# Kernel optimization log

Hardware: AMD Instinct MI355X
Metric: run time of the kernel (lower is better)

Reference implementation:

```python
import jax, jax.numpy as jnp
import numpy as np

B, T, D = 32, 4096, 64
K = 512
COMMITMENT_COST = 0.25


def setup_inputs() -> dict:
    key = jax.random.key(0)
    kz, kw = jax.random.split(key)
    z = jax.random.normal(kz, (B, T, D), dtype=jnp.float32)
    # matches nn.init.uniform_(weight, -1/K, 1/K)
    W = jax.random.uniform(kw, (K, D), dtype=jnp.float32, minval=-1.0 / K, maxval=1.0 / K)
    return {"z": z, "W": W}


def reference(z, W):
    b, t, d = z.shape
    z_flat = z.reshape(-1, d)                                   # [N, D]
    # squared euclidean distances via ||z||^2 + ||w||^2 - 2 z.w
    dist = (jnp.sum(z_flat * z_flat, axis=1, keepdims=True)
            + jnp.sum(W * W, axis=1)
            - 2.0 * z_flat @ W.T)                               # [N, K]
    indices = jnp.argmin(dist, axis=1)                          # [N]
    z_q = W[indices].reshape(b, t, d)                           # gather
    # straight-through estimator
    z_q_st = z + jax.lax.stop_gradient(z_q - z)
    loss = COMMITMENT_COST * jnp.mean((z - jax.lax.stop_gradient(z_q_st)) ** 2)
    return z_q_st, indices.reshape(b, t), loss
```

## Files before the change

### kernel.cpp

```cpp
#include <hip/hip_runtime.h>
#include <hip/hip_bf16.h>
#include <math.h>

#define NROWS 131072
#define KC    512
#define DD    64
#define NELEM (NROWS * DD)

#define OUT_IDX_OFF  NELEM
#define OUT_LOSS_OFF (NELEM + NROWS)

#define MARGIN 3e-5f

#define WSO_CNT   0
#define WSO_DONE  4
#define WSO_LOSS  8
#define WSO_WNORM 64
#define WSO_BH    4096
#define WSO_BL    (WSO_BH + 65536)
#define WSO_LIST  (WSO_BL + 65536)

typedef __attribute__((ext_vector_type(8))) short short8;
typedef __attribute__((ext_vector_type(4))) float f32x4;

__device__ __forceinline__ short f2bf_bits(float f) {
  __hip_bfloat16 h = __float2bfloat16(f);
  short s; __builtin_memcpy(&s, &h, 2); return s;
}
__device__ __forceinline__ float bfbits2f(short s) {
  __hip_bfloat16 h; __builtin_memcpy(&h, &s, 2);
  return __bfloat162float(h);
}
__device__ __forceinline__ void cvt8(const float* __restrict__ p, short8& hi, short8& lo) {
#pragma unroll
  for (int j = 0; j < 8; j++) {
    float f = p[j];
    short hb = f2bf_bits(f);
    float r = f - bfbits2f(hb);
    hi[j] = hb;
    lo[j] = f2bf_bits(r);
  }
}

__device__ __forceinline__ float np_sumsq64(const float* __restrict__ p) {
#pragma clang fp contract(off)
  float r0 = p[0] * p[0], r1 = p[1] * p[1], r2 = p[2] * p[2], r3 = p[3] * p[3];
  float r4 = p[4] * p[4], r5 = p[5] * p[5], r6 = p[6] * p[6], r7 = p[7] * p[7];
  for (int i = 8; i < 64; i += 8) {
    r0 = r0 + p[i + 0] * p[i + 0];
    r1 = r1 + p[i + 1] * p[i + 1];
    r2 = r2 + p[i + 2] * p[i + 2];
    r3 = r3 + p[i + 3] * p[i + 3];
    r4 = r4 + p[i + 4] * p[i + 4];
    r5 = r5 + p[i + 5] * p[i + 5];
    r6 = r6 + p[i + 6] * p[i + 6];
    r7 = r7 + p[i + 7] * p[i + 7];
  }
  return ((r0 + r1) + (r2 + r3)) + ((r4 + r5) + (r6 + r7));
}

__global__ void k_prep(const float* __restrict__ W, short8* __restrict__ Bh,
                       short8* __restrict__ Bl, float* __restrict__ wnorm,
                       int* __restrict__ flagCnt, int* __restrict__ doneCnt,
                       float* __restrict__ lossSum) {
  int gtid = blockIdx.x * blockDim.x + threadIdx.x;
  if (gtid == 0) { *flagCnt = 0; *doneCnt = 0; *lossSum = 0.0f; }
  int t = gtid >> 7, rem = gtid & 127;
  int h = rem >> 6, L = rem & 63;
  int cw = (t << 4) + (L & 15);
  int dbase = (h << 5) + ((L >> 4) << 3);
  short8 hi, lo;
  cvt8(W + (cw << 6) + dbase, hi, lo);
  Bh[gtid] = hi;
  Bl[gtid] = lo;
  if (gtid < KC) wnorm[gtid] = np_sumsq64(W + (gtid << 6));
}

#define MT 2
#define ROWS_PER_WAVE (MT * 16)
#define ROWS_PER_BLOCK (ROWS_PER_WAVE * 4)

__global__ __launch_bounds__(256, 4) void k_screen(
    const float* __restrict__ z, const float* __restrict__ W,
    const short8* __restrict__ Bh, const short8* __restrict__ Bl,
    const float* __restrict__ wnorm, float* __restrict__ out,
    int* __restrict__ flagList, int* __restrict__ flagCnt,
    float* __restrict__ lossSum) {
  const int lane = threadIdx.x & 63;
  const int wave = threadIdx.x >> 6;
  const int rowBase = blockIdx.x * ROWS_PER_BLOCK + wave * ROWS_PER_WAVE;
  const int m = lane & 15, quad = lane >> 4;

  short8 Ah[MT][2], Al[MT][2];
#pragma unroll
  for (int mt = 0; mt < MT; mt++) {
    const float* zp = z + (size_t)(rowBase + (mt << 4) + m) * DD + (quad << 3);
#pragma unroll
    for (int h = 0; h < 2; h++) cvt8(zp + (h << 5), Ah[mt][h], Al[mt][h]);
  }

  float b1[MT][4], b2[MT][4];
  int bi[MT][4];
#pragma unroll
  for (int mt = 0; mt < MT; mt++)
#pragma unroll
    for (int r = 0; r < 4; r++) { b1[mt][r] = 1e30f; b2[mt][r] = 1e30f; bi[mt][r] = 0; }

  short8 cBh[2], cBl[2];
#pragma unroll
  for (int h = 0; h < 2; h++) {
    cBh[h] = Bh[(h << 6) + lane];
    cBl[h] = Bl[(h << 6) + lane];
  }
  float cwn = wnorm[m];

  for (int t = 0; t < 32; t++) {
    const int tn = (t + 1) & 31;
    short8 nBh[2], nBl[2];
#pragma unroll
    for (int h = 0; h < 2; h++) {
      nBh[h] = Bh[(((tn << 1) + h) << 6) + lane];
      nBl[h] = Bl[(((tn << 1) + h) << 6) + lane];
    }
    float nwn = wnorm[(tn << 4) + m];

    f32x4 acc[MT] = {{0.f, 0.f, 0.f, 0.f}, {0.f, 0.f, 0.f, 0.f}};
#pragma unroll
    for (int h = 0; h < 2; h++) {
#pragma unroll
      for (int mt = 0; mt < MT; mt++)
        acc[mt] = __builtin_amdgcn_mfma_f32_16x16x32_bf16(Ah[mt][h], cBh[h], acc[mt], 0, 0, 0);
#pragma unroll
      for (int mt = 0; mt < MT; mt++)
        acc[mt] = __builtin_amdgcn_mfma_f32_16x16x32_bf16(Al[mt][h], cBh[h], acc[mt], 0, 0, 0);
#pragma unroll
      for (int mt = 0; mt < MT; mt++)
        acc[mt] = __builtin_amdgcn_mfma_f32_16x16x32_bf16(Ah[mt][h], cBl[h], acc[mt], 0, 0, 0);
    }

    int colv = (t << 4) + m;
#pragma unroll
    for (int mt = 0; mt < MT; mt++)
#pragma unroll
      for (int r = 0; r < 4; r++) {
        float s = fmaf(-2.0f, acc[mt][r], cwn);
        if (s < b1[mt][r]) { b2[mt][r] = b1[mt][r]; b1[mt][r] = s; bi[mt][r] = colv; }
        else b2[mt][r] = fminf(b2[mt][r], s);
      }

    cBh[0] = nBh[0]; cBh[1] = nBh[1];
    cBl[0] = nBl[0]; cBl[1] = nBl[1];
    cwn = nwn;
  }

#pragma unroll
  for (int off = 1; off < 16; off <<= 1) {
#pragma unroll
    for (int mt = 0; mt < MT; mt++)
#pragma unroll
      for (int r = 0; r < 4; r++) {
        float o1 = __shfl_xor(b1[mt][r], off, 64);
        float o2 = __shfl_xor(b2[mt][r], off, 64);
        int oi = __shfl_xor(bi[mt][r], off, 64);
        if (o1 < b1[mt][r] || (o1 == b1[mt][r] && oi < bi[mt][r])) {
          b2[mt][r] = fminf(b1[mt][r], o2);
          b1[mt][r] = o1; bi[mt][r] = oi;
        } else {
          b2[mt][r] = fminf(b2[mt][r], o1);
        }
      }
  }

  float lossAcc = 0.f;
#pragma unroll
  for (int mt = 0; mt < MT; mt++)
#pragma unroll
    for (int r = 0; r < 4; r++) {
      const int row = rowBase + (mt << 4) + (quad << 2) + r;
      const int ki = bi[mt][r];
      f32x4 zv = *(const f32x4*)(z + (size_t)row * DD + (m << 2));
      f32x4 wv = *(const f32x4*)(W + (ki << 6) + (m << 2));
      f32x4 ov;
#pragma unroll
      for (int j = 0; j < 4; j++) {
        float tt = wv[j] - zv[j];
        ov[j] = zv[j] + tt;
        float dl = zv[j] - ov[j];
        lossAcc = fmaf(dl, dl, lossAcc);
      }
      *(f32x4*)(out + (size_t)row * DD + (m << 2)) = ov;
      if (m == 0) {
        out[OUT_IDX_OFF + row] = (float)ki;
        if (b2[mt][r] - b1[mt][r] < MARGIN) {
          int slot = atomicAdd(flagCnt, 1);
          flagList[slot] = row;
        }
      }
    }

#pragma unroll
  for (int off = 1; off < 64; off <<= 1) lossAcc += __shfl_xor(lossAcc, off, 64);
  if (lane == 0) atomicAdd(lossSum, lossAcc);
}

__global__ void k_refine(const float* __restrict__ z, const float* __restrict__ W,
                         const float* __restrict__ wnp, float* __restrict__ out,
                         const int* __restrict__ flagList,
                         const int* __restrict__ flagCnt,
                         float* __restrict__ lossSum, int* __restrict__ doneCnt) {
  int nflag = *flagCnt;
  int lane = threadIdx.x & 63;
  int wave = (blockIdx.x * blockDim.x + threadIdx.x) >> 6;
  int nWaves = (gridDim.x * blockDim.x) >> 6;

  for (int f = wave; f < nflag; f += nWaves) {
    int row = flagList[f];
    const float* zr = z + (size_t)row * DD;
    float A = np_sumsq64(zr);

    float best = 1e30f;
    int bk = 0x7fffffff;
#pragma unroll
    for (int j = 0; j < KC / 64; j++) {
      int k = lane + (j << 6);
      const float* wk = W + (k << 6);
      double cd = 0.0;
      for (int d = 0; d < DD; d++) cd = fma((double)zr[d], (double)wk[d], cd);
      float twoC = (float)(2.0 * cd);
      float dist;
      {
#pragma clang fp contract(off)
        float t1 = A + wnp[k];
        dist = t1 - twoC;
      }
      if (dist < best || (dist == best && k < bk)) { best = dist; bk = k; }
    }
#pragma unroll
    for (int off = 1; off < 64; off <<= 1) {
      float ov = __shfl_xor(best, off, 64);
      int ok = __shfl_xor(bk, off, 64);
      if (ov < best || (ov == best && ok < bk)) { best = ov; bk = ok; }
    }

    int kold = (int)out[OUT_IDX_OFF + row];
    if (bk != kold) {
      float zv = zr[lane];
      float wN = W[(bk << 6) + lane];
      float oOld = out[(size_t)row * DD + lane];
      float tN = wN - zv;
      float oN = zv + tN;
      out[(size_t)row * DD + lane] = oN;
      float dN = zv - oN, dO = zv - oOld;
      float delta = dN * dN - dO * dO;
#pragma unroll
      for (int off = 1; off < 64; off <<= 1) delta += __shfl_xor(delta, off, 64);
      if (lane == 0) {
        atomicAdd(lossSum, delta);
        out[OUT_IDX_OFF + row] = (float)bk;
      }
    }
  }

  __syncthreads();
  if (threadIdx.x == 0) {
    __threadfence();
    int d = atomicAdd(doneCnt, 1);
    if (d == (int)gridDim.x - 1) {
      float s = atomicAdd(lossSum, 0.0f);
      out[OUT_LOSS_OFF] = 0.25f * s / (float)NELEM;
    }
  }
}

extern "C" void kernel_launch(void* const* d_in, const int* in_sizes, int n_in,
                              void* d_out, int out_size, void* d_ws, size_t ws_size,
                              hipStream_t stream) {
  const float* z = (const float*)d_in[0];
  const float* W = (const float*)d_in[1];
  float* out = (float*)d_out;
  char* ws = (char*)d_ws;

  int* flagCnt = (int*)(ws + WSO_CNT);
  int* doneCnt = (int*)(ws + WSO_DONE);
  float* lossSum = (float*)(ws + WSO_LOSS);
  float* wnorm = (float*)(ws + WSO_WNORM);
  short8* Bh = (short8*)(ws + WSO_BH);
  short8* Bl = (short8*)(ws + WSO_BL);
  int* flagList = (int*)(ws + WSO_LIST);

  k_prep<<<16, 256, 0, stream>>>(W, Bh, Bl, wnorm, flagCnt, doneCnt, lossSum);
  k_screen<<<NROWS / ROWS_PER_BLOCK, 256, 0, stream>>>(z, W, Bh, Bl, wnorm, out,
                                                       flagList, flagCnt, lossSum);
  k_refine<<<256, 256, 0, stream>>>(z, W, wnorm, out, flagList, flagCnt,
                                    lossSum, doneCnt);
}
```

Baseline: 202.8 us.

## Split codebook across waves and share row tile via LDS in screen kernel

Each block now handles 64 rows, staged once into shared memory as hi/lo bf16 fragments. Each of the four waves scans a quarter of the codebook (8 tiles) over all 64 rows, rather than every wave scanning all 512 codes for its own 32 rows. Per-wave best and second-best results are merged through shared memory, and the per-block loss is reduced before a single atomic. This cuts per-wave B-fragment traffic and atomics and raises MT, at the cost of extra syncs, more LDS and register pressure, and a tie-break merge that no longer prefers the lower index on equal distances.

Result: slower. 491.6 us (+142.4%).

```diff
diff --git a/kernel.cpp b/kernel.cpp
--- a/kernel.cpp
+++ b/kernel.cpp
@@ -76,28 +76,52 @@
   if (gtid < KC) wnorm[gtid] = np_sumsq64(W + (gtid << 6));
 }
 
-#define MT 2
-#define ROWS_PER_WAVE (MT * 16)
-#define ROWS_PER_BLOCK (ROWS_PER_WAVE * 4)
-
-__global__ __launch_bounds__(256, 4) void k_screen(
+#define MT 4
+#define ROWS_PER_BLOCK 64
+#define TPW 8
+
+__global__ __launch_bounds__(256, 6) void k_screen(
     const float* __restrict__ z, const float* __restrict__ W,
     const short8* __restrict__ Bh, const short8* __restrict__ Bl,
     const float* __restrict__ wnorm, float* __restrict__ out,
     int* __restrict__ flagList, int* __restrict__ flagCnt,
     float* __restrict__ lossSum) {
-  const int lane = threadIdx.x & 63;
-  const int wave = threadIdx.x >> 6;
-  const int rowBase = blockIdx.x * ROWS_PER_BLOCK + wave * ROWS_PER_WAVE;
+  const int tid = threadIdx.x;
+  const int lane = tid & 63;
+  const int wave = tid >> 6;
+  const int rowBase = blockIdx.x * ROWS_PER_BLOCK;
   const int m = lane & 15, quad = lane >> 4;
 
+  __shared__ short8 sAh[MT * 2][64];
+  __shared__ short8 sAl[MT * 2][64];
+  __shared__ float sb1[4][64], sb2[4][64];
+  __shared__ int   sbi[4][64];
+  __shared__ float lw[4];
+
+  {
+    const int row = tid >> 2;
+    const int colbase = (tid & 3) << 4;
+    const int mt = row >> 4, mm = row & 15;
+    const int h = colbase >> 5;
+    const int q0 = (colbase >> 3) & 3;
+    const float* zp = z + (size_t)(rowBase + row) * DD + colbase;
+    short8 hi0, lo0, hi1, lo1;
+    cvt8(zp, hi0, lo0);
+    cvt8(zp + 8, hi1, lo1);
+    const int f = mt * 2 + h;
+    sAh[f][(q0 << 4) + mm] = hi0;       sAl[f][(q0 << 4) + mm] = lo0;
+    sAh[f][((q0 + 1) << 4) + mm] = hi1; sAl[f][((q0 + 1) << 4) + mm] = lo1;
+  }
+  __syncthreads();
+
   short8 Ah[MT][2], Al[MT][2];
 #pragma unroll
-  for (int mt = 0; mt < MT; mt++) {
-    const float* zp = z + (size_t)(rowBase + (mt << 4) + m) * DD + (quad << 3);
-#pragma unroll
-    for (int h = 0; h < 2; h++) cvt8(zp + (h << 5), Ah[mt][h], Al[mt][h]);
-  }
+  for (int mt = 0; mt < MT; mt++)
+#pragma unroll
+    for (int h = 0; h < 2; h++) {
+      Ah[mt][h] = sAh[mt * 2 + h][lane];
+      Al[mt][h] = sAl[mt * 2 + h][lane];
+    }
 
   float b1[MT][4], b2[MT][4];
   int bi[MT][4];
@@ -106,16 +130,19 @@
 #pragma unroll
     for (int r = 0; r < 4; r++) { b1[mt][r] = 1e30f; b2[mt][r] = 1e30f; bi[mt][r] = 0; }
 
+  const int tbase = wave * TPW;
   short8 cBh[2], cBl[2];
 #pragma unroll
   for (int h = 0; h < 2; h++) {
-    cBh[h] = Bh[(h << 6) + lane];
-    cBl[h] = Bl[(h << 6) + lane];
-  }
-  float cwn = wnorm[m];
-
-  for (int t = 0; t < 32; t++) {
-    const int tn = (t + 1) & 31;
+    cBh[h] = Bh[(((tbase << 1) + h) << 6) + lane];
+    cBl[h] = Bl[(((tbase << 1) + h) << 6) + lane];
+  }
+  float cwn = wnorm[(tbase << 4) + m];
+
+#pragma unroll
+  for (int tl = 0; tl < TPW; tl++) {
+    const int t = tbase + tl;
+    const int tn = tbase + ((tl + 1) & (TPW - 1));
     short8 nBh[2], nBl[2];
 #pragma unroll
     for (int h = 0; h < 2; h++) {
@@ -124,7 +151,8 @@
     }
     float nwn = wnorm[(tn << 4) + m];
 
-    f32x4 acc[MT] = {{0.f, 0.f, 0.f, 0.f}, {0.f, 0.f, 0.f, 0.f}};
+    f32x4 acc[MT] = {{0.f, 0.f, 0.f, 0.f}, {0.f, 0.f, 0.f, 0.f},
+                     {0.f, 0.f, 0.f, 0.f}, {0.f, 0.f, 0.f, 0.f}};
 #pragma unroll
     for (int h = 0; h < 2; h++) {
 #pragma unroll
@@ -138,7 +166,7 @@
         acc[mt] = __builtin_amdgcn_mfma_f32_16x16x32_bf16(Ah[mt][h], cBl[h], acc[mt], 0, 0, 0);
     }
 
-    int colv = (t << 4) + m;
+    const int colv = (t << 4) + m;
 #pragma unroll
     for (int mt = 0; mt < MT; mt++)
 #pragma unroll
@@ -171,36 +199,62 @@
       }
   }
 
+  if (m == 0) {
+#pragma unroll
+    for (int mt = 0; mt < MT; mt++)
+#pragma unroll
+      for (int r = 0; r < 4; r++) {
+        const int rl = (mt << 4) + (quad << 2) + r;
+        sb1[wave][rl] = b1[mt][r];
+        sb2[wave][rl] = b2[mt][r];
+        sbi[wave][rl] = bi[mt][r];
+      }
+  }
+  __syncthreads();
+
+  const int rl = (wave << 4) + m;
+  float B1 = sb1[0][rl], B2 = sb2[0][rl];
+  int KI = sbi[0][rl];
+#pragma unroll
+  for (int w2 = 1; w2 < 4; w2++) {
+    float o1 = sb1[w2][rl], o2 = sb2[w2][rl];
+    int oi = sbi[w2][rl];
+    if (o1 < B1) { B2 = fminf(B1, o2); B1 = o1; KI = oi; }
+    else B2 = fminf(B2, o1);
+  }
+  if (lane < 16) {
+    const int row = rowBase + rl;
+    out[OUT_IDX_OFF + row] = (float)KI;
+    if (B2 - B1 < MARGIN) {
+      int slot = atomicAdd(flagCnt, 1);
+      flagList[slot] = row;
+    }
+  }
+
   float lossAcc = 0.f;
 #pragma unroll
-  for (int mt = 0; mt < MT; mt++)
-#pragma unroll
-    for (int r = 0; r < 4; r++) {
-      const int row = rowBase + (mt << 4) + (quad << 2) + r;
-      const int ki = bi[mt][r];
-      f32x4 zv = *(const f32x4*)(z + (size_t)row * DD + (m << 2));
-      f32x4 wv = *(const f32x4*)(W + (ki << 6) + (m << 2));
-      f32x4 ov;
-#pragma unroll
-      for (int j = 0; j < 4; j++) {
-        float tt = wv[j] - zv[j];
-        ov[j] = zv[j] + tt;
-        float dl = zv[j] - ov[j];
-        lossAcc = fmaf(dl, dl, lossAcc);
-      }
-      *(f32x4*)(out + (size_t)row * DD + (m << 2)) = ov;
-      if (m == 0) {
-        out[OUT_IDX_OFF + row] = (float)ki;
-        if (b2[mt][r] - b1[mt][r] < MARGIN) {
-          int slot = atomicAdd(flagCnt, 1);
-          flagList[slot] = row;
-        }
-      }
-    }
+  for (int sub = 0; sub < 4; sub++) {
+    const int ro = (sub << 2) + quad;
+    const int row = rowBase + (wave << 4) + ro;
+    const int kr = __shfl(KI, ro, 64);
+    f32x4 zv = *(const f32x4*)(z + (size_t)row * DD + (m << 2));
+    f32x4 wv = *(const f32x4*)(W + (kr << 6) + (m << 2));
+    f32x4 ov;
+#pragma unroll
+    for (int j = 0; j < 4; j++) {
+      float tt = wv[j] - zv[j];
+      ov[j] = zv[j] + tt;
+      float dl = zv[j] - ov[j];
+      lossAcc = fmaf(dl, dl, lossAcc);
+    }
+    *(f32x4*)(out + (size_t)row * DD + (m << 2)) = ov;
+  }
 
 #pragma unroll
   for (int off = 1; off < 64; off <<= 1) lossAcc += __shfl_xor(lossAcc, off, 64);
-  if (lane == 0) atomicAdd(lossSum, lossAcc);
+  if (lane == 0) lw[wave] = lossAcc;
+  __syncthreads();
+  if (tid == 0) atomicAdd(lossSum, (lw[0] + lw[1]) + (lw[2] + lw[3]));
 }
 
 __global__ void k_refine(const float* __restrict__ z, const float* __restrict__ W,
```

## Pre-split z into bf16 MFMA fragments and stage codebook in LDS

Applied to the files above, without the earlier changes.

Adds a k_prep_z kernel that converts z into hi/lo bf16 fragments laid out for MFMA and stores them in the output buffer as scratch. k_screen then loads those fragments directly, and uses 512-thread blocks that stage half the codebook fragments into shared memory per phase instead of streaming them from global memory each tile. The aim is to cut repeated global codebook reads and per-row conversion work. In exchange it adds an extra kernel launch and a full write and read of the z fragments, and it relies on the screen kernel's writes to out not clobbering fragments other blocks still need.

New measurement: 203.2 us. No clear change (+0.2%).

```diff
diff --git a/kernel.cpp b/kernel.cpp
--- a/kernel.cpp
+++ b/kernel.cpp
@@ -76,28 +76,48 @@
   if (gtid < KC) wnorm[gtid] = np_sumsq64(W + (gtid << 6));
 }
 
+__global__ void k_prep_z(const float* __restrict__ z, short8* __restrict__ Af) {
+  int gtid = blockIdx.x * blockDim.x + threadIdx.x;
+  int r16 = gtid >> 7, rem = gtid & 127;
+  int h = rem >> 6, L = rem & 63;
+  const float* zp = z + ((size_t)((r16 << 4) + (L & 15)) << 6) + (h << 5) + ((L >> 4) << 3);
+  short8 hi, lo;
+  cvt8(zp, hi, lo);
+  size_t F = ((size_t)(r16 << 1) + h) << 1;
+  Af[F * 64 + L] = hi;
+  Af[(F + 1) * 64 + L] = lo;
+}
+
 #define MT 2
-#define ROWS_PER_WAVE (MT * 16)
-#define ROWS_PER_BLOCK (ROWS_PER_WAVE * 4)
-
-__global__ __launch_bounds__(256, 4) void k_screen(
+#define ROWS_PER_WAVE 32
+#define ROWS_PER_BLOCK 256
+#define SCREEN_THREADS 512
+
+__global__ __launch_bounds__(SCREEN_THREADS, 4) void k_screen(
     const float* __restrict__ z, const float* __restrict__ W,
     const short8* __restrict__ Bh, const short8* __restrict__ Bl,
-    const float* __restrict__ wnorm, float* __restrict__ out,
+    const float* __restrict__ wnorm, float* out,
     int* __restrict__ flagList, int* __restrict__ flagCnt,
     float* __restrict__ lossSum) {
-  const int lane = threadIdx.x & 63;
-  const int wave = threadIdx.x >> 6;
+  const int tid = threadIdx.x;
+  const int lane = tid & 63;
+  const int wave = tid >> 6;
+  const int m = lane & 15, quad = lane >> 4;
   const int rowBase = blockIdx.x * ROWS_PER_BLOCK + wave * ROWS_PER_WAVE;
-  const int m = lane & 15, quad = lane >> 4;
-
+  const int r16base = rowBase >> 4;
+
+  __shared__ short8 sB[4096];
+
+  const short8* Af = (const short8*)out;
   short8 Ah[MT][2], Al[MT][2];
 #pragma unroll
-  for (int mt = 0; mt < MT; mt++) {
-    const float* zp = z + (size_t)(rowBase + (mt << 4) + m) * DD + (quad << 3);
-#pragma unroll
-    for (int h = 0; h < 2; h++) cvt8(zp + (h << 5), Ah[mt][h], Al[mt][h]);
-  }
+  for (int mt = 0; mt < MT; mt++)
+#pragma unroll
+    for (int h = 0; h < 2; h++) {
+      const size_t F = ((size_t)((r16base + mt) << 1) + h) << 1;
+      Ah[mt][h] = Af[F * 64 + lane];
+      Al[mt][h] = Af[(F + 1) * 64 + lane];
+    }
 
   float b1[MT][4], b2[MT][4];
   int bi[MT][4];
@@ -106,51 +126,51 @@
 #pragma unroll
     for (int r = 0; r < 4; r++) { b1[mt][r] = 1e30f; b2[mt][r] = 1e30f; bi[mt][r] = 0; }
 
-  short8 cBh[2], cBl[2];
-#pragma unroll
-  for (int h = 0; h < 2; h++) {
-    cBh[h] = Bh[(h << 6) + lane];
-    cBl[h] = Bl[(h << 6) + lane];
-  }
-  float cwn = wnorm[m];
-
-  for (int t = 0; t < 32; t++) {
-    const int tn = (t + 1) & 31;
-    short8 nBh[2], nBl[2];
-#pragma unroll
-    for (int h = 0; h < 2; h++) {
-      nBh[h] = Bh[(((tn << 1) + h) << 6) + lane];
-      nBl[h] = Bl[(((tn << 1) + h) << 6) + lane];
-    }
-    float nwn = wnorm[(tn << 4) + m];
-
-    f32x4 acc[MT] = {{0.f, 0.f, 0.f, 0.f}, {0.f, 0.f, 0.f, 0.f}};
-#pragma unroll
-    for (int h = 0; h < 2; h++) {
+  for (int ph = 0; ph < 2; ph++) {
+    if (ph) __syncthreads();
+#pragma unroll
+    for (int c = 0; c < 4; c++) {
+      const int i = (c << 9) + tid;
+      sB[i] = Bh[(ph << 11) + i];
+      sB[2048 + i] = Bl[(ph << 11) + i];
+    }
+    __syncthreads();
+
+#pragma unroll 2
+    for (int tl = 0; tl < 16; tl++) {
+      const int t = (ph << 4) + tl;
+      short8 Bhf[2], Blf[2];
+#pragma unroll
+      for (int h = 0; h < 2; h++) {
+        Bhf[h] = sB[(((tl << 1) + h) << 6) + lane];
+        Blf[h] = sB[2048 + (((tl << 1) + h) << 6) + lane];
+      }
+      const float wn = wnorm[(t << 4) + m];
+
+      f32x4 acc[MT] = {{0.f, 0.f, 0.f, 0.f}, {0.f, 0.f, 0.f, 0.f}};
+#pragma unroll
+      for (int h = 0; h < 2; h++) {
+#pragma unroll
+        for (int mt = 0; mt < MT; mt++)
+          acc[mt] = __builtin_amdgcn_mfma_f32_16x16x32_bf16(Ah[mt][h], Bhf[h], acc[mt], 0, 0, 0);
+#pragma unroll
+        for (int mt = 0; mt < MT; mt++)
+          acc[mt] = __builtin_amdgcn_mfma_f32_16x16x32_bf16(Al[mt][h], Bhf[h], acc[mt], 0, 0, 0);
+#pragma unroll
+        for (int mt = 0; mt < MT; mt++)
+          acc[mt] = __builtin_amdgcn_mfma_f32_16x16x32_bf16(Ah[mt][h], Blf[h], acc[mt], 0, 0, 0);
+      }
+
+      const int colv = (t << 4) + m;
 #pragma unroll
       for (int mt = 0; mt < MT; mt++)
-        acc[mt] = __builtin_amdgcn_mfma_f32_16x16x32_bf16(Ah[mt][h], cBh[h], acc[mt], 0, 0, 0);
-#pragma unroll
-      for (int mt = 0; mt < MT; mt++)
-        acc[mt] = __builtin_amdgcn_mfma_f32_16x16x32_bf16(Al[mt][h], cBh[h], acc[mt], 0, 0, 0);
-#pragma unroll
-      for (int mt = 0; mt < MT; mt++)
-        acc[mt] = __builtin_amdgcn_mfma_f32_16x16x32_bf16(Ah[mt][h], cBl[h], acc[mt], 0, 0, 0);
-    }
-
-    int colv = (t << 4) + m;
-#pragma unroll
-    for (int mt = 0; mt < MT; mt++)
-#pragma unroll
-      for (int r = 0; r < 4; r++) {
-        float s = fmaf(-2.0f, acc[mt][r], cwn);
-        if (s < b1[mt][r]) { b2[mt][r] = b1[mt][r]; b1[mt][r] = s; bi[mt][r] = colv; }
-        else b2[mt][r] = fminf(b2[mt][r], s);
-      }
-
-    cBh[0] = nBh[0]; cBh[1] = nBh[1];
-    cBl[0] = nBl[0]; cBl[1] = nBl[1];
-    cwn = nwn;
+#pragma unroll
+        for (int r = 0; r < 4; r++) {
+          float s = fmaf(-2.0f, acc[mt][r], wn);
+          if (s < b1[mt][r]) { b2[mt][r] = b1[mt][r]; b1[mt][r] = s; bi[mt][r] = colv; }
+          else b2[mt][r] = fminf(b2[mt][r], s);
+        }
+    }
   }
 
 #pragma unroll
@@ -289,8 +309,9 @@
   int* flagList = (int*)(ws + WSO_LIST);
 
   k_prep<<<16, 256, 0, stream>>>(W, Bh, Bl, wnorm, flagCnt, doneCnt, lossSum);
-  k_screen<<<NROWS / ROWS_PER_BLOCK, 256, 0, stream>>>(z, W, Bh, Bl, wnorm, out,
-                                                       flagList, flagCnt, lossSum);
+  k_prep_z<<<4096, 256, 0, stream>>>(z, (short8*)out);
+  k_screen<<<NROWS / ROWS_PER_BLOCK, SCREEN_THREADS, 0, stream>>>(
+      z, W, Bh, Bl, wnorm, out, flagList, flagCnt, lossSum);
   k_refine<<<256, 256, 0, stream>>>(z, W, wnorm, out, flagList, flagCnt,
                                     lossSum, doneCnt);
 }
```

## Fuse refine pass into screen kernel with per-block flag lists

Applied to the files above, without the earlier changes.

Folds the exact fp64 refinement of near-tie rows into the screening kernel. Flagged rows now go into a shared-memory list per block instead of a global atomic list, and each block's waves re-check them right after screening. The screen tile grows from 2 to 4 row tiles per wave, which removes the software prefetch of B fragments, and a transposed copy of W is built in prep so refinement loads are coalesced across lanes. This removes one kernel launch and the global atomics, at the cost of higher register pressure from the larger tiles and possible load imbalance when a block has many flagged rows.

Measured after the change: 193.3 us. -4.7%, faster.

```diff
diff --git a/kernel.cpp b/kernel.cpp
--- a/kernel.cpp
+++ b/kernel.cpp
@@ -12,13 +12,12 @@
 
 #define MARGIN 3e-5f
 
-#define WSO_CNT   0
 #define WSO_DONE  4
 #define WSO_LOSS  8
 #define WSO_WNORM 64
 #define WSO_BH    4096
 #define WSO_BL    (WSO_BH + 65536)
-#define WSO_LIST  (WSO_BL + 65536)
+#define WSO_WT    (WSO_BL + 65536)
 
 typedef __attribute__((ext_vector_type(8))) short short8;
 typedef __attribute__((ext_vector_type(4))) float f32x4;
@@ -61,10 +60,10 @@
 
 __global__ void k_prep(const float* __restrict__ W, short8* __restrict__ Bh,
                        short8* __restrict__ Bl, float* __restrict__ wnorm,
-                       int* __restrict__ flagCnt, int* __restrict__ doneCnt,
-                       float* __restrict__ lossSum) {
+                       float* __restrict__ Wt,
+                       int* __restrict__ doneCnt, float* __restrict__ lossSum) {
   int gtid = blockIdx.x * blockDim.x + threadIdx.x;
-  if (gtid == 0) { *flagCnt = 0; *doneCnt = 0; *lossSum = 0.0f; }
+  if (gtid == 0) { *doneCnt = 0; *lossSum = 0.0f; }
   int t = gtid >> 7, rem = gtid & 127;
   int h = rem >> 6, L = rem & 63;
   int cw = (t << 4) + (L & 15);
@@ -74,23 +73,35 @@
   Bh[gtid] = hi;
   Bl[gtid] = lo;
   if (gtid < KC) wnorm[gtid] = np_sumsq64(W + (gtid << 6));
-}
-
-#define MT 2
-#define ROWS_PER_WAVE (MT * 16)
-#define ROWS_PER_BLOCK (ROWS_PER_WAVE * 4)
-
-__global__ __launch_bounds__(256, 4) void k_screen(
+#pragma unroll
+  for (int c = 0; c < 8; c++) {
+    int idx = (c << 12) + gtid;
+    int d = idx >> 9, k = idx & 511;
+    Wt[idx] = W[(k << 6) + d];
+  }
+}
+
+#define MT 4
+#define ROWS_PER_WAVE 64
+#define ROWS_PER_BLOCK 256
+
+__global__ __launch_bounds__(256) void k_screen(
     const float* __restrict__ z, const float* __restrict__ W,
     const short8* __restrict__ Bh, const short8* __restrict__ Bl,
-    const float* __restrict__ wnorm, float* __restrict__ out,
-    int* __restrict__ flagList, int* __restrict__ flagCnt,
-    float* __restrict__ lossSum) {
-  const int lane = threadIdx.x & 63;
-  const int wave = threadIdx.x >> 6;
+    const float* __restrict__ wnorm, const float* __restrict__ Wt,
+    float* __restrict__ out,
+    float* __restrict__ lossSum, int* __restrict__ doneCnt) {
+  const int tid = threadIdx.x;
+  const int lane = tid & 63;
+  const int wave = tid >> 6;
   const int rowBase = blockIdx.x * ROWS_PER_BLOCK + wave * ROWS_PER_WAVE;
   const int m = lane & 15, quad = lane >> 4;
 
+  __shared__ int fcnt;
+  __shared__ int fl[ROWS_PER_BLOCK];
+  __shared__ float lw[4];
+  if (tid == 0) fcnt = 0;
+
   short8 Ah[MT][2], Al[MT][2];
 #pragma unroll
   for (int mt = 0; mt < MT; mt++) {
@@ -98,6 +109,7 @@
 #pragma unroll
     for (int h = 0; h < 2; h++) cvt8(zp + (h << 5), Ah[mt][h], Al[mt][h]);
   }
+  __syncthreads();
 
   float b1[MT][4], b2[MT][4];
   int bi[MT][4];
@@ -106,57 +118,45 @@
 #pragma unroll
     for (int r = 0; r < 4; r++) { b1[mt][r] = 1e30f; b2[mt][r] = 1e30f; bi[mt][r] = 0; }
 
-  short8 cBh[2], cBl[2];
-#pragma unroll
-  for (int h = 0; h < 2; h++) {
-    cBh[h] = Bh[(h << 6) + lane];
-    cBl[h] = Bl[(h << 6) + lane];
-  }
-  float cwn = wnorm[m];
-
   for (int t = 0; t < 32; t++) {
-    const int tn = (t + 1) & 31;
-    short8 nBh[2], nBl[2];
+    short8 Bhf[2], Blf[2];
 #pragma unroll
     for (int h = 0; h < 2; h++) {
-      nBh[h] = Bh[(((tn << 1) + h) << 6) + lane];
-      nBl[h] = Bl[(((tn << 1) + h) << 6) + lane];
-    }
-    float nwn = wnorm[(tn << 4) + m];
-
-    f32x4 acc[MT] = {{0.f, 0.f, 0.f, 0.f}, {0.f, 0.f, 0.f, 0.f}};
+      Bhf[h] = Bh[((t * 2 + h) << 6) + lane];
+      Blf[h] = Bl[((t * 2 + h) << 6) + lane];
+    }
+    float wn = wnorm[(t << 4) + m];
+
+    f32x4 acc[4] = {{0.f, 0.f, 0.f, 0.f}, {0.f, 0.f, 0.f, 0.f},
+                    {0.f, 0.f, 0.f, 0.f}, {0.f, 0.f, 0.f, 0.f}};
 #pragma unroll
     for (int h = 0; h < 2; h++) {
 #pragma unroll
-      for (int mt = 0; mt < MT; mt++)
-        acc[mt] = __builtin_amdgcn_mfma_f32_16x16x32_bf16(Ah[mt][h], cBh[h], acc[mt], 0, 0, 0);
-#pragma unroll
-      for (int mt = 0; mt < MT; mt++)
-        acc[mt] = __builtin_amdgcn_mfma_f32_16x16x32_bf16(Al[mt][h], cBh[h], acc[mt], 0, 0, 0);
-#pragma unroll
-      for (int mt = 0; mt < MT; mt++)
-        acc[mt] = __builtin_amdgcn_mfma_f32_16x16x32_bf16(Ah[mt][h], cBl[h], acc[mt], 0, 0, 0);
+      for (int mt = 0; mt < 4; mt++)
+        acc[mt] = __builtin_amdgcn_mfma_f32_16x16x32_bf16(Ah[mt][h], Bhf[h], acc[mt], 0, 0, 0);
+#pragma unroll
+      for (int mt = 0; mt < 4; mt++)
+        acc[mt] = __builtin_amdgcn_mfma_f32_16x16x32_bf16(Al[mt][h], Bhf[h], acc[mt], 0, 0, 0);
+#pragma unroll
+      for (int mt = 0; mt < 4; mt++)
+        acc[mt] = __builtin_amdgcn_mfma_f32_16x16x32_bf16(Ah[mt][h], Blf[h], acc[mt], 0, 0, 0);
     }
 
     int colv = (t << 4) + m;
 #pragma unroll
-    for (int mt = 0; mt < MT; mt++)
+    for (int mt = 0; mt < 4; mt++)
 #pragma unroll
       for (int r = 0; r < 4; r++) {
-        float s = fmaf(-2.0f, acc[mt][r], cwn);
+        float s = fmaf(-2.0f, acc[mt][r], wn);
         if (s < b1[mt][r]) { b2[mt][r] = b1[mt][r]; b1[mt][r] = s; bi[mt][r] = colv; }
         else b2[mt][r] = fminf(b2[mt][r], s);
       }
-
-    cBh[0] = nBh[0]; cBh[1] = nBh[1];
-    cBl[0] = nBl[0]; cBl[1] = nBl[1];
-    cwn = nwn;
   }
 
 #pragma unroll
   for (int off = 1; off < 16; off <<= 1) {
 #pragma unroll
-    for (int mt = 0; mt < MT; mt++)
+    for (int mt = 0; mt < 4; mt++)
 #pragma unroll
       for (int r = 0; r < 4; r++) {
         float o1 = __shfl_xor(b1[mt][r], off, 64);
@@ -192,29 +192,21 @@
       if (m == 0) {
         out[OUT_IDX_OFF + row] = (float)ki;
         if (b2[mt][r] - b1[mt][r] < MARGIN) {
-          int slot = atomicAdd(flagCnt, 1);
-          flagList[slot] = row;
+          int slot = atomicAdd(&fcnt, 1);
+          fl[slot] = row;
         }
       }
     }
 
 #pragma unroll
   for (int off = 1; off < 64; off <<= 1) lossAcc += __shfl_xor(lossAcc, off, 64);
-  if (lane == 0) atomicAdd(lossSum, lossAcc);
-}
-
-__global__ void k_refine(const float* __restrict__ z, const float* __restrict__ W,
-                         const float* __restrict__ wnp, float* __restrict__ out,
-                         const int* __restrict__ flagList,
-                         const int* __restrict__ flagCnt,
-                         float* __restrict__ lossSum, int* __restrict__ doneCnt) {
-  int nflag = *flagCnt;
-  int lane = threadIdx.x & 63;
-  int wave = (blockIdx.x * blockDim.x + threadIdx.x) >> 6;
-  int nWaves = (gridDim.x * blockDim.x) >> 6;
-
-  for (int f = wave; f < nflag; f += nWaves) {
-    int row = flagList[f];
+  if (lane == 0) lw[wave] = lossAcc;
+  __syncthreads();
+  if (tid == 0) atomicAdd(lossSum, (lw[0] + lw[1]) + (lw[2] + lw[3]));
+
+  const int nf = fcnt;
+  for (int f = wave; f < nf; f += 4) {
+    const int row = fl[f];
     const float* zr = z + (size_t)row * DD;
     float A = np_sumsq64(zr);
 
@@ -223,14 +215,14 @@
 #pragma unroll
     for (int j = 0; j < KC / 64; j++) {
       int k = lane + (j << 6);
-      const float* wk = W + (k << 6);
       double cd = 0.0;
-      for (int d = 0; d < DD; d++) cd = fma((double)zr[d], (double)wk[d], cd);
+      for (int d = 0; d < DD; d++)
+        cd = fma((double)zr[d], (double)Wt[(d << 9) + k], cd);
       float twoC = (float)(2.0 * cd);
       float dist;
       {
 #pragma clang fp contract(off)
-        float t1 = A + wnp[k];
+        float t1 = A + wnorm[k];
         dist = t1 - twoC;
       }
       if (dist < best || (dist == best && k < bk)) { best = dist; bk = k; }
@@ -262,10 +254,10 @@
   }
 
   __syncthreads();
-  if (threadIdx.x == 0) {
+  if (tid == 0) {
     __threadfence();
-    int d = atomicAdd(doneCnt, 1);
-    if (d == (int)gridDim.x - 1) {
+    int dnum = atomicAdd(doneCnt, 1);
+    if (dnum == (int)gridDim.x - 1) {
       float s = atomicAdd(lossSum, 0.0f);
       out[OUT_LOSS_OFF] = 0.25f * s / (float)NELEM;
     }
@@ -280,17 +272,14 @@
   float* out = (float*)d_out;
   char* ws = (char*)d_ws;
 
-  int* flagCnt = (int*)(ws + WSO_CNT);
   int* doneCnt = (int*)(ws + WSO_DONE);
   float* lossSum = (float*)(ws + WSO_LOSS);
   float* wnorm = (float*)(ws + WSO_WNORM);
   short8* Bh = (short8*)(ws + WSO_BH);
   short8* Bl = (short8*)(ws + WSO_BL);
-  int* flagList = (int*)(ws + WSO_LIST);
-
-  k_prep<<<16, 256, 0, stream>>>(W, Bh, Bl, wnorm, flagCnt, doneCnt, lossSum);
-  k_screen<<<NROWS / ROWS_PER_BLOCK, 256, 0, stream>>>(z, W, Bh, Bl, wnorm, out,
-                                                       flagList, flagCnt, lossSum);
-  k_refine<<<256, 256, 0, stream>>>(z, W, wnorm, out, flagList, flagCnt,
-                                    lossSum, doneCnt);
-}
+  float* Wt = (float*)(ws + WSO_WT);
+
+  k_prep<<<16, 256, 0, stream>>>(W, Bh, Bl, wnorm, Wt, doneCnt, lossSum);
+  k_screen<<<NROWS / ROWS_PER_BLOCK, 256, 0, stream>>>(
+      z, W, Bh, Bl, wnorm, Wt, out, lossSum, doneCnt);
+}
```
